# Optimization experiments

Hardware: AMD Instinct MI355X
Metric: run time of the kernel (lower is better)

The kernel has to match this reference:

```python
import jax, jax.numpy as jnp
import numpy as np

N, E, H, C = 20000, 320000, 4, 64
F_NODE, F_EDGE, F_W, T, LH = 64, 16, 8, 24, 64
NEG_SLOPE, EPS = 0.2, 1e-5


def setup_inputs() -> dict:
    key = jax.random.key(0)
    ks = jax.random.split(key, 20)
    d = {
        'node_static_features': jax.random.normal(ks[0], (N, F_NODE), jnp.float32),
        'edge_static_features': jax.random.normal(ks[1], (E, F_EDGE), jnp.float32),
        'node_dynamic_features': jax.random.normal(ks[2], (N, T, F_W), jnp.float32),
        'edge_index': jax.random.randint(ks[3], (E, 2), 0, N, jnp.int64),
        # GATConv params (PyG layout): shared lin for src/dst, lin_edge, att vectors, bias
        'W_lin': jax.random.normal(ks[4], (F_NODE, H * C), jnp.float32) / np.sqrt(F_NODE),
        'W_edge': jax.random.normal(ks[5], (F_EDGE, H * C), jnp.float32) / np.sqrt(F_EDGE),
        'att_src': jax.random.normal(ks[6], (H, C), jnp.float32) / np.sqrt(C),
        'att_dst': jax.random.normal(ks[7], (H, C), jnp.float32) / np.sqrt(C),
        'att_edge': jax.random.normal(ks[8], (H, C), jnp.float32) / np.sqrt(C),
        'gat_bias': jnp.zeros((C,), jnp.float32),
        # BatchNorm
        'bn_gamma': jnp.ones((C,), jnp.float32),
        'bn_beta': jnp.zeros((C,), jnp.float32),
        # LSTM (torch gate order i,f,g,o)
        'W_ih': jax.random.normal(ks[9], (4 * LH, F_W), jnp.float32) / np.sqrt(F_W),
        'W_hh': jax.random.normal(ks[10], (4 * LH, LH), jnp.float32) / np.sqrt(LH),
        'b_ih': jnp.zeros((4 * LH,), jnp.float32),
        'b_hh': jnp.zeros((4 * LH,), jnp.float32),
        # MLP head
        'W_hid': jax.random.normal(ks[11], (C + LH, C // 2), jnp.float32) / np.sqrt(C + LH),
        'b_hid': jnp.zeros((C // 2,), jnp.float32),
        'W_out': jax.random.normal(ks[12], (C // 2, 1), jnp.float32) / np.sqrt(C // 2),
        'b_out': jnp.zeros((1,), jnp.float32),
    }
    return d


def _gat_forward(x, edge_attr, src, dst, W_lin, W_edge, att_src, att_dst, att_edge, gat_bias):
    # add self loops with edge_attr fill_value='mean' (per-target mean of incoming edge feats)
    deg = jax.ops.segment_sum(jnp.ones((src.shape[0],), x.dtype), dst, num_segments=N)
    mean_attr = jax.ops.segment_sum(edge_attr, dst, num_segments=N) / jnp.maximum(deg, 1.0)[:, None]
    loop = jnp.arange(N, dtype=src.dtype)
    src = jnp.concatenate([src, loop]); dst = jnp.concatenate([dst, loop])
    edge_attr = jnp.concatenate([edge_attr, mean_attr], axis=0)  # [E+N, F_EDGE]

    xh = (x @ W_lin).reshape(N, H, C)                              # [N,H,C]
    eh = (edge_attr @ W_edge).reshape(-1, H, C)                    # [E+N,H,C]
    a_src = jnp.einsum('nhc,hc->nh', xh, att_src)                  # [N,H]
    a_dst = jnp.einsum('nhc,hc->nh', xh, att_dst)
    a_edge = jnp.einsum('ehc,hc->eh', eh, att_edge)
    alpha = a_src[src] + a_dst[dst] + a_edge                       # [E+N,H]
    alpha = jax.nn.leaky_relu(alpha, NEG_SLOPE)
    # segment softmax over edges grouped by destination node
    amax = jax.ops.segment_max(alpha, dst, num_segments=N)
    amax = jnp.where(jnp.isfinite(amax), amax, 0.0)
    ex = jnp.exp(alpha - amax[dst])
    denom = jax.ops.segment_sum(ex, dst, num_segments=N)
    attn = ex / (denom[dst] + 1e-16)                               # [E+N,H]
    msg = xh[src] * attn[:, :, None]                               # [E+N,H,C]
    out = jax.ops.segment_sum(msg, dst, num_segments=N)            # [N,H,C]
    return out.mean(axis=1) + gat_bias                             # concat=False -> head mean


def _lstm_last(xs, W_ih, W_hh, b_ih, b_hh):
    # xs: [N, T, F_W]; returns h_T: [N, LH]
    def step(carry, x_t):
        h, c = carry
        g = x_t @ W_ih.T + b_ih + h @ W_hh.T + b_hh
        i, f, gg, o = jnp.split(g, 4, axis=-1)
        c = jax.nn.sigmoid(f) * c + jax.nn.sigmoid(i) * jnp.tanh(gg)
        h = jax.nn.sigmoid(o) * jnp.tanh(c)
        return (h, c), None
    h0 = jnp.zeros((xs.shape[0], LH), xs.dtype)
    (h, _), _ = jax.lax.scan(step, (h0, h0), jnp.swapaxes(xs, 0, 1))
    return h


def reference(node_static_features, edge_static_features, node_dynamic_features, edge_index,
              W_lin, W_edge, att_src, att_dst, att_edge, gat_bias,
              bn_gamma, bn_beta, W_ih, W_hh, b_ih, b_hh,
              W_hid, b_hid, W_out, b_out):
    src, dst = edge_index[:, 0], edge_index[:, 1]
    x1 = _gat_forward(node_static_features, edge_static_features, src, dst,
                      W_lin, W_edge, att_src, att_dst, att_edge, gat_bias)
    # BatchNorm1d (training-mode batch stats) + relu; dropout is identity at eval
    mu = x1.mean(axis=0)
    var = x1.var(axis=0)
    x1 = jax.nn.relu((x1 - mu) / jnp.sqrt(var + EPS) * bn_gamma + bn_beta)
    h_last = _lstm_last(node_dynamic_features, W_ih, W_hh, b_ih, b_hh)  # [N,LH]
    combined = jnp.concatenate([x1, h_last], axis=1)
    hidden = jax.nn.relu(combined @ W_hid + b_hid)
    return hidden @ W_out + b_out  # [N,1]
```

## Files before the change

### kernel.cpp

```cpp
#include <hip/hip_runtime.h>
#include <hip/hip_bf16.h>

constexpr int N_  = 20000;
constexpr int E_  = 320000;
constexpr int T_  = 24;
constexpr float NEG_ = 0.2f;
constexpr float EPS_ = 1e-5f;
constexpr int MAXD_ = 128;
constexpr int LNB_ = 8;

typedef __attribute__((ext_vector_type(8)))  short short8v;
typedef __attribute__((ext_vector_type(16))) float f32x16;

__device__ __forceinline__ int esrc(const int* __restrict__ p, int e, int f64) {
    return f64 ? p[4 * e] : p[2 * e];
}
__device__ __forceinline__ int edst(const int* __restrict__ p, int e, int f64) {
    return f64 ? p[4 * e + 2] : p[2 * e + 1];
}

__device__ __forceinline__ float sigf(float x) {
    return __builtin_amdgcn_rcpf(1.f + __expf(-x));
}
__device__ __forceinline__ float tanhfast(float x) {
    return 1.f - 2.f * __builtin_amdgcn_rcpf(1.f + __expf(2.f * x));
}

__device__ __forceinline__ short f2bf(float f) {
    union { float f; unsigned u; } v; v.f = f;
    unsigned r = v.u + 0x7FFFu + ((v.u >> 16) & 1u);
    return (short)(r >> 16);
}

__global__ void k_detect(const int* __restrict__ idx, int* __restrict__ flag) {
    int v = idx[2 * threadIdx.x + 1];
    unsigned long long b = __ballot(v != 0);
    if (threadIdx.x == 0) flag[0] = (b == 0ULL) ? 1 : 0;
}

__global__ __launch_bounds__(256) void k_Pq(
    const float* __restrict__ W_edge, const float* __restrict__ att_edge,
    const float* __restrict__ att_src, const float* __restrict__ att_dst,
    const float* __restrict__ W_lin, float* __restrict__ P, float* __restrict__ Q) {
    int t = threadIdx.x;
    if (t < 64) {
        int k = t >> 2, h = t & 3;
        float s = 0.f;
        for (int c = 0; c < 64; ++c) s += W_edge[k * 256 + h * 64 + c] * att_edge[h * 64 + c];
        P[k * 4 + h] = s;
    }
    {
        int k = t >> 2, h = t & 3;
        float s = 0.f, d = 0.f;
        for (int c = 0; c < 64; ++c) {
            float w = W_lin[k * 256 + h * 64 + c];
            s += w * att_src[h * 64 + c];
            d += w * att_dst[h * 64 + c];
        }
        Q[k * 8 + h] = s;
        Q[k * 8 + 4 + h] = d;
    }
}

__global__ __launch_bounds__(256) void k_node(
    const float* __restrict__ x, const float* __restrict__ W_lin,
    const float* __restrict__ Q,
    float* __restrict__ xh, float* __restrict__ asrc, float* __restrict__ adst) {
    __shared__ float xs[16][65];
    __shared__ float Qsh[64][8];
    int t = threadIdx.x;
    int nb = blockIdx.x * 16;
    for (int i = t; i < 16 * 64; i += 256) xs[i >> 6][i & 63] = x[(long)nb * 64 + i];
    for (int i = t; i < 64 * 8; i += 256) ((float*)Qsh)[i] = Q[i];
    __syncthreads();
    float acc[16];
#pragma unroll
    for (int m = 0; m < 16; ++m) acc[m] = 0.f;
    for (int k = 0; k < 64; ++k) {
        float w = W_lin[k * 256 + t];
#pragma unroll
        for (int m = 0; m < 16; ++m) acc[m] += xs[m][k] * w;
    }
#pragma unroll
    for (int m = 0; m < 16; ++m) xh[(long)(nb + m) * 256 + t] = acc[m];
    if (t < 128) {
        int m = t >> 3, q = t & 7;
        float s = 0.f;
        for (int k = 0; k < 64; ++k) s += xs[m][k] * Qsh[k][q];
        if (q < 4) asrc[(nb + m) * 4 + q] = s;
        else       adst[(nb + m) * 4 + (q - 4)] = s;
    }
}

__global__ __launch_bounds__(256) void k_e1(
    const int* __restrict__ idx, const int* __restrict__ flag,
    const float* __restrict__ ea, const float* __restrict__ P,
    float4* __restrict__ aebuf, int* __restrict__ degi) {
    __shared__ float Ps[256];
    int t = threadIdx.x;
    if (t < 64) Ps[t] = P[t];
    __syncthreads();
    int e = blockIdx.x * 256 + t;
    if (e >= E_) return;
    int f64 = flag[0];
    int d = edst(idx, e, f64);
    const float* ep = ea + (long)e * 16;
    float ae[4] = {0.f, 0.f, 0.f, 0.f};
#pragma unroll
    for (int k = 0; k < 16; ++k) {
        float v = ep[k];
#pragma unroll
        for (int h = 0; h < 4; ++h) ae[h] += v * Ps[k * 4 + h];
    }
    aebuf[e] = make_float4(ae[0], ae[1], ae[2], ae[3]);
    atomicAdd(&degi[d], 1);
}

__global__ __launch_bounds__(256) void k_scan(const int* __restrict__ degi,
                                              int* __restrict__ offs) {
    __shared__ int part[256];
    int t = threadIdx.x;
    int base = t * 80;
    int s = 0;
    for (int i = 0; i < 80; ++i) { int ix = base + i; if (ix < N_) s += degi[ix]; }
    part[t] = s;
    __syncthreads();
    for (int d = 1; d < 256; d <<= 1) {
        int v = (t >= d) ? part[t - d] : 0;
        __syncthreads();
        part[t] += v;
        __syncthreads();
    }
    int run = (t > 0) ? part[t - 1] : 0;
    for (int i = 0; i < 80; ++i) {
        int ix = base + i;
        if (ix < N_) { offs[ix] = run; run += degi[ix]; }
    }
}

__global__ __launch_bounds__(256) void k_e2(
    const int* __restrict__ idx, const int* __restrict__ flag,
    const int* __restrict__ offs, int* __restrict__ cursor,
    int2* __restrict__ csr) {
    int e = blockIdx.x * 256 + threadIdx.x;
    if (e >= E_) return;
    int f64 = flag[0];
    int d = edst(idx, e, f64);
    int s = esrc(idx, e, f64);
    int pos = atomicAdd(&cursor[d], 1);
    csr[offs[d] + pos] = make_int2(e, s);
}

__global__ __launch_bounds__(256) void k_n2(
    const int* __restrict__ offs, const int* __restrict__ degi,
    const int2* __restrict__ csr, const float4* __restrict__ aebuf,
    const float4* __restrict__ asrc4, const float4* __restrict__ adst4,
    const float* __restrict__ xh, const float* __restrict__ gat_bias,
    float* __restrict__ x1) {
    __shared__ int   sS[4][MAXD_];
    __shared__ float4 sEx[4][MAXD_];
    int t = threadIdx.x, w = t >> 6, lane = t & 63;
    int n = blockIdx.x * 4 + w;
    if (n >= N_) return;
    int deg = degi[n], off = offs[n];
    float4 ad = adst4[n];

    float4 aesum = make_float4(0, 0, 0, 0), den = make_float4(0, 0, 0, 0);
    for (int base = 0; base < deg; base += 64) {
        int i = base + lane;
        if (i < deg) {
            int2 pr = csr[off + i];
            float4 ae = aebuf[pr.x];
            float4 as = asrc4[pr.y];
            float a0 = as.x + ad.x + ae.x; a0 = a0 > 0.f ? a0 : NEG_ * a0;
            float a1 = as.y + ad.y + ae.y; a1 = a1 > 0.f ? a1 : NEG_ * a1;
            float a2 = as.z + ad.z + ae.z; a2 = a2 > 0.f ? a2 : NEG_ * a2;
            float a3 = as.w + ad.w + ae.w; a3 = a3 > 0.f ? a3 : NEG_ * a3;
            float4 ex = make_float4(__expf(a0), __expf(a1), __expf(a2), __expf(a3));
            aesum.x += ae.x; aesum.y += ae.y; aesum.z += ae.z; aesum.w += ae.w;
            den.x += ex.x; den.y += ex.y; den.z += ex.z; den.w += ex.w;
            if (i < MAXD_) { sS[w][i] = pr.y; sEx[w][i] = ex; }
        }
    }
#pragma unroll
    for (int m = 32; m >= 1; m >>= 1) {
        aesum.x += __shfl_xor(aesum.x, m); aesum.y += __shfl_xor(aesum.y, m);
        aesum.z += __shfl_xor(aesum.z, m); aesum.w += __shfl_xor(aesum.w, m);
        den.x += __shfl_xor(den.x, m); den.y += __shfl_xor(den.y, m);
        den.z += __shfl_xor(den.z, m); den.w += __shfl_xor(den.w, m);
    }
    float dv = fmaxf((float)deg, 1.f);
    float4 as = asrc4[n];
    float a0 = as.x + ad.x + aesum.x / dv; a0 = a0 > 0.f ? a0 : NEG_ * a0;
    float a1 = as.y + ad.y + aesum.y / dv; a1 = a1 > 0.f ? a1 : NEG_ * a1;
    float a2 = as.z + ad.z + aesum.z / dv; a2 = a2 > 0.f ? a2 : NEG_ * a2;
    float a3 = as.w + ad.w + aesum.w / dv; a3 = a3 > 0.f ? a3 : NEG_ * a3;
    float4 exs = make_float4(__expf(a0), __expf(a1), __expf(a2), __expf(a3));
    den.x += exs.x; den.y += exs.y; den.z += exs.z; den.w += exs.w;
    float i0 = 1.f / (den.x + 1e-16f), i1 = 1.f / (den.y + 1e-16f);
    float i2 = 1.f / (den.z + 1e-16f), i3 = 1.f / (den.w + 1e-16f);
    __syncthreads();

    float acc = 0.f;
    for (int i = 0; i < deg; ++i) {
        int s; float4 ex;
        if (i < MAXD_) { s = sS[w][i]; ex = sEx[w][i]; }
        else {
            int2 pr = csr[off + i];
            s = pr.y;
            float4 ae = aebuf[pr.x];
            float4 a5 = asrc4[s];
            float b0 = a5.x + ad.x + ae.x; b0 = b0 > 0.f ? b0 : NEG_ * b0;
            float b1 = a5.y + ad.y + ae.y; b1 = b1 > 0.f ? b1 : NEG_ * b1;
            float b2 = a5.z + ad.z + ae.z; b2 = b2 > 0.f ? b2 : NEG_ * b2;
            float b3 = a5.w + ad.w + ae.w; b3 = b3 > 0.f ? b3 : NEG_ * b3;
            ex = make_float4(__expf(b0), __expf(b1), __expf(b2), __expf(b3));
        }
        const float* xp = xh + (long)s * 256;
        acc += ex.x * i0 * xp[lane] + ex.y * i1 * xp[64 + lane]
             + ex.z * i2 * xp[128 + lane] + ex.w * i3 * xp[192 + lane];
    }
    {
        const float* xp = xh + (long)n * 256;
        acc += exs.x * i0 * xp[lane] + exs.y * i1 * xp[64 + lane]
             + exs.z * i2 * xp[128 + lane] + exs.w * i3 * xp[192 + lane];
    }
    x1[(long)n * 64 + lane] = acc * 0.25f + gat_bias[lane];
}

__global__ __launch_bounds__(256) void k_x1stats(
    const float* __restrict__ x1, float* __restrict__ bnsum) {
    int c = threadIdx.x & 63, r = threadIdx.x >> 6;
    float s = 0.f, s2 = 0.f;
    for (int n = blockIdx.x * 4 + r; n < N_; n += gridDim.x * 4) {
        float v = x1[(long)n * 64 + c];
        s += v; s2 += v * v;
    }
    __shared__ float red[4][128];
    red[r][c] = s; red[r][64 + c] = s2;
    __syncthreads();
    if (r == 0) {
        float ts = red[0][c] + red[1][c] + red[2][c] + red[3][c];
        float t2 = red[0][64 + c] + red[1][64 + c] + red[2][64 + c] + red[3][64 + c];
        atomicAdd(&bnsum[c], ts);
        atomicAdd(&bnsum[64 + c], t2);
    }
}

__global__ void k_bnfin(const float* __restrict__ bnsum, const float* __restrict__ gamma,
                        const float* __restrict__ beta, float* __restrict__ bnp) {
    int c = threadIdx.x;
    float mu = bnsum[c] / (float)N_;
    float var = bnsum[64 + c] / (float)N_ - mu * mu;
    float sc = gamma[c] * rsqrtf(var + EPS_);
    bnp[c] = sc;
    bnp[64 + c] = beta[c] - mu * sc;
}

__global__ __launch_bounds__(64, 1) void k_lstm_mfma(
    const float* __restrict__ xdyn, const float* __restrict__ W_ih,
    const float* __restrict__ W_hh, const float* __restrict__ b_ih,
    const float* __restrict__ b_hh, float* __restrict__ hlast) {
    __shared__ short Hl[32 * 64];
    char* Hb = (char*)Hl;
    const int l = threadIdx.x;
    const int lm = l & 31;
    const int g  = l >> 5;
    const int nbase = blockIdx.x * LNB_;

    short8v Bh[8][4];
#pragma unroll
    for (int t8 = 0; t8 < 8; ++t8) {
#pragma unroll
        for (int ks = 0; ks < 4; ++ks) {
            int j = 32 * t8 + lm;
            const float* wp = W_hh + j * 64 + 16 * ks + 8 * g;
            float4 wa = *(const float4*)wp;
            float4 wb = *(const float4*)(wp + 4);
            short8v f;
            f[0] = f2bf(wa.x); f[1] = f2bf(wa.y); f[2] = f2bf(wa.z); f[3] = f2bf(wa.w);
            f[4] = f2bf(wb.x); f[5] = f2bf(wb.y); f[6] = f2bf(wb.z); f[7] = f2bf(wb.w);
            Bh[t8][ks] = f;
        }
    }
    short8v B2[8];
#pragma unroll
    for (int t8 = 0; t8 < 8; ++t8) {
        int j = 32 * t8 + lm;
        short8v f;
        if (g == 0) {
            const float* wp = W_ih + j * 8;
            float4 wa = *(const float4*)wp;
            float4 wb = *(const float4*)(wp + 4);
            f[0] = f2bf(wa.x); f[1] = f2bf(wa.y); f[2] = f2bf(wa.z); f[3] = f2bf(wa.w);
            f[4] = f2bf(wb.x); f[5] = f2bf(wb.y); f[6] = f2bf(wb.z); f[7] = f2bf(wb.w);
        } else {
#pragma unroll
            for (int e = 0; e < 8; ++e) f[e] = 0;
            f[0] = f2bf(b_ih[j] + b_hh[j]);
        }
        B2[t8] = f;
    }
    short8v xAc;
#pragma unroll
    for (int e = 0; e < 8; ++e) xAc[e] = 0;
    xAc[0] = (short)0x3F80;

    f32x16 zc;
#pragma unroll
    for (int e = 0; e < 16; ++e) zc[e] = 0.f;

    {
        short8v zv;
#pragma unroll
        for (int e = 0; e < 8; ++e) zv[e] = 0;
#pragma unroll
        for (int i = l; i < 256; i += 64) ((short8v*)Hl)[i] = zv;
    }
    float cst[2][4];
#pragma unroll
    for (int jt = 0; jt < 2; ++jt)
#pragma unroll
        for (int r = 0; r < 4; ++r) cst[jt][r] = 0.f;

    __syncthreads();

    const bool xld = (g == 0) && (lm < LNB_);
    const float* xbase = xdyn + (long)(nbase + (lm & (LNB_ - 1))) * T_ * 8;
    float4 xp0 = make_float4(0, 0, 0, 0), xp1 = make_float4(0, 0, 0, 0);
    if (xld) { xp0 = *(const float4*)xbase; xp1 = *(const float4*)(xbase + 4); }

    for (int t = 0; t < T_; ++t) {
        short8v xA;
        if (g == 0) {
            if (xld) {
                xA[0] = f2bf(xp0.x); xA[1] = f2bf(xp0.y); xA[2] = f2bf(xp0.z); xA[3] = f2bf(xp0.w);
                xA[4] = f2bf(xp1.x); xA[5] = f2bf(xp1.y); xA[6] = f2bf(xp1.z); xA[7] = f2bf(xp1.w);
                if (t < T_ - 1) {
                    xp0 = *(const float4*)(xbase + (t + 1) * 8);
                    xp1 = *(const float4*)(xbase + (t + 1) * 8 + 4);
                }
            } else {
#pragma unroll
                for (int e = 0; e < 8; ++e) xA[e] = 0;
            }
        } else xA = xAc;

        f32x16 acc[8];
#pragma unroll
        for (int t8 = 0; t8 < 8; ++t8)
            acc[t8] = __builtin_amdgcn_mfma_f32_32x32x16_bf16(xA, B2[t8], zc, 0, 0, 0);

        short8v hA[4];
#pragma unroll
        for (int ks = 0; ks < 4; ++ks) {
            int raddr = (lm * 128 + 32 * ks + 16 * g) ^ ((lm & 7) << 4);
            hA[ks] = *(const short8v*)(Hb + raddr);
        }
#pragma unroll
        for (int ks = 0; ks < 4; ++ks)
#pragma unroll
            for (int t8 = 0; t8 < 8; ++t8)
                acc[t8] = __builtin_amdgcn_mfma_f32_32x32x16_bf16(hA[ks], Bh[t8][ks], acc[t8], 0, 0, 0);

        __syncthreads();

#pragma unroll
        for (int jt = 0; jt < 2; ++jt) {
#pragma unroll
            for (int r = 0; r < 4; ++r) {
                float iv = acc[jt][r];
                float fv = acc[2 + jt][r];
                float gv = acc[4 + jt][r];
                float ov = acc[6 + jt][r];
                float si = sigf(iv), sf = sigf(fv), tg = tanhfast(gv), so = sigf(ov);
                float cn = sf * cst[jt][r] + si * tg;
                cst[jt][r] = cn;
                float hn = so * tanhfast(cn);
                int mrow = r + 4 * g;
                int j = 32 * jt + lm;
                int waddr = (mrow * 128 + j * 2) ^ ((mrow & 7) << 4);
                *(short*)(Hb + waddr) = f2bf(hn);
                if (t == T_ - 1) hlast[(long)(nbase + mrow) * 64 + j] = hn;
            }
        }
        __syncthreads();
    }
}

__global__ __launch_bounds__(256) void k_head(
    const float* __restrict__ x1, const float* __restrict__ hlast,
    const float* __restrict__ bnp, const float* __restrict__ W_hid,
    const float* __restrict__ b_hid, const float* __restrict__ W_out,
    const float* __restrict__ b_out, float* __restrict__ out) {
    int n = blockIdx.x * 256 + threadIdx.x;
    if (n >= N_) return;
    float comb[128];
#pragma unroll
    for (int i = 0; i < 64; ++i)
        comb[i] = fmaxf(x1[(long)n * 64 + i] * bnp[i] + bnp[64 + i], 0.f);
#pragma unroll
    for (int i = 0; i < 64; ++i) comb[64 + i] = hlast[(long)n * 64 + i];
    float o = b_out[0];
    for (int j = 0; j < 32; ++j) {
        float a = b_hid[j];
#pragma unroll
        for (int i = 0; i < 128; ++i) a += comb[i] * W_hid[i * 32 + j];
        o += fmaxf(a, 0.f) * W_out[j];
    }
    out[n] = o;
}

extern "C" void kernel_launch(void* const* d_in, const int* in_sizes, int n_in,
                              void* d_out, int out_size, void* d_ws, size_t ws_size,
                              hipStream_t stream) {
    const float* x_node   = (const float*)d_in[0];
    const float* ea       = (const float*)d_in[1];
    const float* xdyn     = (const float*)d_in[2];
    const int*   eidx     = (const int*)d_in[3];
    const float* W_lin    = (const float*)d_in[4];
    const float* W_edge   = (const float*)d_in[5];
    const float* att_src  = (const float*)d_in[6];
    const float* att_dst  = (const float*)d_in[7];
    const float* att_edge = (const float*)d_in[8];
    const float* gat_bias = (const float*)d_in[9];
    const float* bn_gamma = (const float*)d_in[10];
    const float* bn_beta  = (const float*)d_in[11];
    const float* W_ih     = (const float*)d_in[12];
    const float* W_hh     = (const float*)d_in[13];
    const float* b_ih     = (const float*)d_in[14];
    const float* b_hh     = (const float*)d_in[15];
    const float* W_hid    = (const float*)d_in[16];
    const float* b_hid    = (const float*)d_in[17];
    const float* W_out    = (const float*)d_in[18];
    const float* b_out    = (const float*)d_in[19];
    float* out = (float*)d_out;

    char* ws = (char*)d_ws;
    size_t off = 0;
    auto alloc = [&](size_t bytes) -> void* {
        void* p = ws + off;
        off = (off + bytes + 255) & ~(size_t)255;
        return p;
    };
    int*      flag  = (int*)alloc(4);
    float*    P     = (float*)alloc(256 * 4);
    float*    Q     = (float*)alloc(64 * 8 * 4);
    float*    bnp   = (float*)alloc(128 * 4);
    char*     zs    = ws + off;
    float*    bnsum = (float*)alloc(128 * 4);
    int*      degi  = (int*)alloc((size_t)N_ * 4);
    int*      cursor= (int*)alloc((size_t)N_ * 4);
    size_t zbytes = (size_t)((ws + off) - zs);
    int*      offs  = (int*)alloc((size_t)N_ * 4);
    float4*   aebuf = (float4*)alloc((size_t)E_ * 16);
    int2*     csr   = (int2*)alloc((size_t)E_ * 8);
    float*    xh    = (float*)alloc((size_t)N_ * 256 * 4);
    float*    asrc  = (float*)alloc((size_t)N_ * 4 * 4);
    float*    adst  = (float*)alloc((size_t)N_ * 4 * 4);
    float*    x1    = (float*)alloc((size_t)N_ * 64 * 4);
    float*    hlast = (float*)alloc((size_t)N_ * 64 * 4);
    (void)ws_size; (void)in_sizes; (void)n_in; (void)out_size;

    hipMemsetAsync(zs, 0, zbytes, stream);
    k_detect<<<1, 64, 0, stream>>>(eidx, flag);
    k_Pq<<<1, 256, 0, stream>>>(W_edge, att_edge, att_src, att_dst, W_lin, P, Q);
    k_node<<<N_ / 16, 256, 0, stream>>>(x_node, W_lin, Q, xh, asrc, adst);
    k_e1<<<(E_ + 255) / 256, 256, 0, stream>>>(eidx, flag, ea, P, aebuf, degi);
    k_scan<<<1, 256, 0, stream>>>(degi, offs);
    k_e2<<<(E_ + 255) / 256, 256, 0, stream>>>(eidx, flag, offs, cursor, csr);
    k_n2<<<(N_ + 3) / 4, 256, 0, stream>>>(offs, degi, csr, aebuf,
                                           (const float4*)asrc, (const float4*)adst,
                                           xh, gat_bias, x1);
    k_x1stats<<<128, 256, 0, stream>>>(x1, bnsum);
    k_bnfin<<<1, 64, 0, stream>>>(bnsum, bn_gamma, bn_beta, bnp);
    k_lstm_mfma<<<(N_ + LNB_ - 1) / LNB_, 64, 0, stream>>>(xdyn, W_ih, W_hh, b_ih, b_hh, hlast);
    k_head<<<(N_ + 255) / 256, 256, 0, stream>>>(x1, hlast, bnp, W_hid, b_hid, W_out, b_out, out);
}
```

Measured before the change: 469.7 us.

## Share LSTM weights in LDS across four waves and drop per-step barriers

The LSTM kernel now runs four independent waves per 256-thread block, each handling 8 nodes. The bf16 W_hh and W_ih/bias fragments are staged once per block in LDS and reread on every MFMA, instead of being held in registers by each single-wave block. Each wave gets its own private hidden-state LDS buffer, so the two per-timestep __syncthreads are removed. The aim is to cut register pressure and raise occupancy, at the cost of extra LDS read traffic every timestep and a reliance on intra-wave LDS ordering being correct without a barrier.

```diff
diff --git a/kernel.cpp b/kernel.cpp
--- a/kernel.cpp
+++ b/kernel.cpp
@@ -257,38 +257,32 @@
     bnp[64 + c] = beta[c] - mu * sc;
 }
 
-__global__ __launch_bounds__(64, 1) void k_lstm_mfma(
+__global__ __launch_bounds__(256, 2) void k_lstm_mfma(
     const float* __restrict__ xdyn, const float* __restrict__ W_ih,
     const float* __restrict__ W_hh, const float* __restrict__ b_ih,
     const float* __restrict__ b_hh, float* __restrict__ hlast) {
-    __shared__ short Hl[32 * 64];
-    char* Hb = (char*)Hl;
-    const int l = threadIdx.x;
-    const int lm = l & 31;
-    const int g  = l >> 5;
-    const int nbase = blockIdx.x * LNB_;
-
-    short8v Bh[8][4];
-#pragma unroll
-    for (int t8 = 0; t8 < 8; ++t8) {
-#pragma unroll
-        for (int ks = 0; ks < 4; ++ks) {
-            int j = 32 * t8 + lm;
-            const float* wp = W_hh + j * 64 + 16 * ks + 8 * g;
-            float4 wa = *(const float4*)wp;
-            float4 wb = *(const float4*)(wp + 4);
-            short8v f;
-            f[0] = f2bf(wa.x); f[1] = f2bf(wa.y); f[2] = f2bf(wa.z); f[3] = f2bf(wa.w);
-            f[4] = f2bf(wb.x); f[5] = f2bf(wb.y); f[6] = f2bf(wb.z); f[7] = f2bf(wb.w);
-            Bh[t8][ks] = f;
-        }
-    }
-    short8v B2[8];
-#pragma unroll
-    for (int t8 = 0; t8 < 8; ++t8) {
-        int j = 32 * t8 + lm;
+    __shared__ char lds[57344];
+    char* W2b = lds + 32768;
+    int t = threadIdx.x;
+    int w = t >> 6, l = t & 63;
+    int lm = l & 31, g = l >> 5;
+
+    for (int idx = t; idx < 2048; idx += 256) {
+        int ll = idx & 63, ks = (idx >> 6) & 3, t8 = idx >> 8;
+        int j = 32 * t8 + (ll & 31);
+        const float* wp = W_hh + j * 64 + 16 * ks + 8 * (ll >> 5);
+        float4 wa = *(const float4*)wp;
+        float4 wb = *(const float4*)(wp + 4);
         short8v f;
-        if (g == 0) {
+        f[0] = f2bf(wa.x); f[1] = f2bf(wa.y); f[2] = f2bf(wa.z); f[3] = f2bf(wa.w);
+        f[4] = f2bf(wb.x); f[5] = f2bf(wb.y); f[6] = f2bf(wb.z); f[7] = f2bf(wb.w);
+        *(short8v*)(lds + idx * 16) = f;
+    }
+    for (int idx = t; idx < 512; idx += 256) {
+        int ll = idx & 63, t8 = idx >> 6;
+        int j = 32 * t8 + (ll & 31);
+        short8v f;
+        if (ll < 32) {
             const float* wp = W_ih + j * 8;
             float4 wa = *(const float4*)wp;
             float4 wb = *(const float4*)(wp + 4);
@@ -299,46 +293,46 @@
             for (int e = 0; e < 8; ++e) f[e] = 0;
             f[0] = f2bf(b_ih[j] + b_hh[j]);
         }
-        B2[t8] = f;
-    }
+        *(short8v*)(W2b + idx * 16) = f;
+    }
+    char* Hb = lds + 40960 + w * 4096;
+    {
+        short8v zv;
+#pragma unroll
+        for (int e = 0; e < 8; ++e) zv[e] = 0;
+#pragma unroll
+        for (int i = l; i < 256; i += 64) ((short8v*)Hb)[i] = zv;
+    }
+    __syncthreads();
+
+    const int nbase = blockIdx.x * 32 + w * LNB_;
+    f32x16 zc;
+#pragma unroll
+    for (int e = 0; e < 16; ++e) zc[e] = 0.f;
     short8v xAc;
 #pragma unroll
     for (int e = 0; e < 8; ++e) xAc[e] = 0;
     xAc[0] = (short)0x3F80;
-
-    f32x16 zc;
-#pragma unroll
-    for (int e = 0; e < 16; ++e) zc[e] = 0.f;
-
-    {
-        short8v zv;
-#pragma unroll
-        for (int e = 0; e < 8; ++e) zv[e] = 0;
-#pragma unroll
-        for (int i = l; i < 256; i += 64) ((short8v*)Hl)[i] = zv;
-    }
     float cst[2][4];
 #pragma unroll
     for (int jt = 0; jt < 2; ++jt)
 #pragma unroll
         for (int r = 0; r < 4; ++r) cst[jt][r] = 0.f;
-
-    __syncthreads();
 
     const bool xld = (g == 0) && (lm < LNB_);
     const float* xbase = xdyn + (long)(nbase + (lm & (LNB_ - 1))) * T_ * 8;
     float4 xp0 = make_float4(0, 0, 0, 0), xp1 = make_float4(0, 0, 0, 0);
     if (xld) { xp0 = *(const float4*)xbase; xp1 = *(const float4*)(xbase + 4); }
 
-    for (int t = 0; t < T_; ++t) {
+    for (int t_ = 0; t_ < T_; ++t_) {
         short8v xA;
         if (g == 0) {
             if (xld) {
                 xA[0] = f2bf(xp0.x); xA[1] = f2bf(xp0.y); xA[2] = f2bf(xp0.z); xA[3] = f2bf(xp0.w);
                 xA[4] = f2bf(xp1.x); xA[5] = f2bf(xp1.y); xA[6] = f2bf(xp1.z); xA[7] = f2bf(xp1.w);
-                if (t < T_ - 1) {
-                    xp0 = *(const float4*)(xbase + (t + 1) * 8);
-                    xp1 = *(const float4*)(xbase + (t + 1) * 8 + 4);
+                if (t_ < T_ - 1) {
+                    xp0 = *(const float4*)(xbase + (t_ + 1) * 8);
+                    xp1 = *(const float4*)(xbase + (t_ + 1) * 8 + 4);
                 }
             } else {
 #pragma unroll
@@ -346,24 +340,26 @@
             }
         } else xA = xAc;
 
-        f32x16 acc[8];
-#pragma unroll
-        for (int t8 = 0; t8 < 8; ++t8)
-            acc[t8] = __builtin_amdgcn_mfma_f32_32x32x16_bf16(xA, B2[t8], zc, 0, 0, 0);
-
         short8v hA[4];
 #pragma unroll
         for (int ks = 0; ks < 4; ++ks) {
             int raddr = (lm * 128 + 32 * ks + 16 * g) ^ ((lm & 7) << 4);
             hA[ks] = *(const short8v*)(Hb + raddr);
         }
+
+        f32x16 acc[8];
+#pragma unroll
+        for (int t8 = 0; t8 < 8; ++t8) {
+            short8v b2f = *(const short8v*)(W2b + (t8 * 64 + l) * 16);
+            acc[t8] = __builtin_amdgcn_mfma_f32_32x32x16_bf16(xA, b2f, zc, 0, 0, 0);
+        }
 #pragma unroll
         for (int ks = 0; ks < 4; ++ks)
 #pragma unroll
-            for (int t8 = 0; t8 < 8; ++t8)
-                acc[t8] = __builtin_amdgcn_mfma_f32_32x32x16_bf16(hA[ks], Bh[t8][ks], acc[t8], 0, 0, 0);
-
-        __syncthreads();
+            for (int t8 = 0; t8 < 8; ++t8) {
+                short8v bh = *(const short8v*)(lds + ((t8 * 4 + ks) * 64 + l) * 16);
+                acc[t8] = __builtin_amdgcn_mfma_f32_32x32x16_bf16(hA[ks], bh, acc[t8], 0, 0, 0);
+            }
 
 #pragma unroll
         for (int jt = 0; jt < 2; ++jt) {
@@ -381,10 +377,9 @@
                 int j = 32 * jt + lm;
                 int waddr = (mrow * 128 + j * 2) ^ ((mrow & 7) << 4);
                 *(short*)(Hb + waddr) = f2bf(hn);
-                if (t == T_ - 1) hlast[(long)(nbase + mrow) * 64 + j] = hn;
+                if (t_ == T_ - 1) hlast[(long)(nbase + mrow) * 64 + j] = hn;
             }
         }
-        __syncthreads();
     }
 }
 
@@ -474,6 +469,6 @@
                                            xh, gat_bias, x1);
     k_x1stats<<<128, 256, 0, stream>>>(x1, bnsum);
     k_bnfin<<<1, 64, 0, stream>>>(bnsum, bn_gamma, bn_beta, bnp);
-    k_lstm_mfma<<<(N_ + LNB_ - 1) / LNB_, 64, 0, stream>>>(xdyn, W_ih, W_hh, b_ih, b_hh, hlast);
+    k_lstm_mfma<<<N_ / 32, 256, 0, stream>>>(xdyn, W_ih, W_hh, b_ih, b_hh, hlast);
     k_head<<<(N_ + 255) / 256, 256, 0, stream>>>(x1, hlast, bnp, W_hid, b_hid, W_out, b_out, out);
 }
```

New measurement: 428.4 us. 1.1x faster.
